# Optimization experiments

Hardware: AMD Instinct MI355X
Metric: run time of the kernel (lower is better)

## Reference

```python
import jax, jax.numpy as jnp
import numpy as np

BS, NUM_PATCH, N_VARS, PATCH_LEN, D_MODEL = 32, 64, 321, 12, 128
TIME_RATIO, FREQ_RATIO = 0.5, 0.4


def setup_inputs() -> dict:
    key = jax.random.key(0)
    ks = jax.random.split(key, 7)
    x = jax.random.normal(ks[0], (BS, NUM_PATCH, N_VARS, PATCH_LEN), jnp.float32)
    W_in = jax.random.normal(ks[1], (PATCH_LEN, D_MODEL), jnp.float32) / np.sqrt(PATCH_LEN)
    b_in = jnp.zeros((D_MODEL,), jnp.float32)
    W_out = jax.random.normal(ks[2], (D_MODEL, PATCH_LEN), jnp.float32) / np.sqrt(D_MODEL)
    b_out = jnp.zeros((PATCH_LEN,), jnp.float32)
    # nn.Parameter(torch.zeros(1,1,1)) in the original; use small random scalars so grads are non-trivial
    time_mask_token = jax.random.normal(ks[3], (), jnp.float32) * 0.02
    freq_mask_token = jax.random.normal(ks[4], (), jnp.float32) * 0.02
    return {"x": x, "W_in": W_in, "b_in": b_in, "W_out": W_out, "b_out": b_out,
            "time_mask_token": time_mask_token, "freq_mask_token": freq_mask_token}


def _scatter_mask(idx, num_patch):
    # idx: [bs, n_vars, k] patch indices to mask (set False). Returns bool [bs, num_patch, n_vars].
    bs, nv, k = idx.shape
    m = jnp.ones((bs, num_patch, nv), dtype=bool)
    b = jnp.arange(bs)[:, None, None]
    v = jnp.arange(nv)[None, :, None]
    return m.at[b, idx, v].set(False)


def reference(x, W_in, b_in, W_out, b_out, time_mask_token, freq_mask_token):
    bs, num_patch, n_vars, patch_len = x.shape

    # patch2emb applied per token (equivalent to the gather-encode path since the
    # projection is pointwise per patch): [bs, np, nv, d_model]
    emb = jnp.einsum('bpvl,ld->bpvd', x, W_in) + b_in

    # ---- time masking: mask patches with highest coefficient of variation ----
    cv = jnp.std(x, axis=-1, ddof=1) / (jnp.mean(x, axis=-1) + 1e-6)  # [bs, np, nv]
    k_t = int(num_patch * TIME_RATIO)
    _, idx_t = jax.lax.top_k(jnp.transpose(cv, (0, 2, 1)), k_t)       # [bs, nv, k_t]
    mask_t = _scatter_mask(idx_t, num_patch)                           # True = keep
    tokens_t = jnp.where(mask_t[..., None], emb, time_mask_token)
    out_t = jnp.einsum('bpvd,dl->bpvl', tokens_t, W_out) + b_out

    # ---- freq masking: mask patches with lowest mean FFT magnitude ----
    mag = jnp.abs(jnp.fft.rfft(x, axis=-1))                            # [bs, np, nv, pl//2+1]
    score = mag.mean(axis=-1)                                          # [bs, np, nv]
    k_f = int(num_patch * FREQ_RATIO)
    _, idx_f = jax.lax.top_k(-jnp.transpose(score, (0, 2, 1)), k_f)    # smallest scores
    mask_f = _scatter_mask(idx_f, num_patch)
    tokens_f = jnp.where(mask_f[..., None], emb, freq_mask_token)
    out_f = jnp.einsum('bpvd,dl->bpvl', tokens_f, W_out) + b_out

    return out_t * 0.5 + out_f * 0.5
```

## Files before the change

### kernel.cpp

```cpp
#include <hip/hip_runtime.h>
#include <math.h>

constexpr int BS = 32, NV = 321, PL = 12, DM = 128;
constexpr int KT = 32;
constexpr int KF = 25;
constexpr int VB = 8;
constexpr int NCHUNK = 41;
constexpr int SST = 72;
constexpr int TOTPV = BS * 64 * NV;
constexpr int MASK_BYTE_OFF = 4096;

__device__ __forceinline__ unsigned ord(float f) {
  unsigned u = __float_as_uint(f);
  return ((int)u < 0) ? ~u : (u | 0x80000000u);
}

__global__ __launch_bounds__(512, 8) void score_kernel(
    const float* __restrict__ x, const float* __restrict__ W_in,
    const float* __restrict__ b_in, const float* __restrict__ W_out,
    const float* __restrict__ b_out, const float* __restrict__ tt,
    const float* __restrict__ ft, float* __restrict__ ws) {
  const int t = threadIdx.x;
  const int chunk = blockIdx.x;
  const int b = blockIdx.y;

  if (chunk == NCHUNK) {
    if (b != 0) return;
    if (t < 144) {
      const int l = t / 12, i = t % 12;
      const float4* Wi = (const float4*)(W_in + i * DM);
      float s = 0.f;
#pragma unroll 8
      for (int d4 = 0; d4 < 32; ++d4) {
        float4 a = Wi[d4];
        const float* wo = W_out + d4 * 48 + l;
        s += a.x * wo[0] + a.y * wo[12] + a.z * wo[24] + a.w * wo[36];
      }
      ws[t] = s;
    } else if (t < 168) {
      const int l = (t - 144) % 12;
      float cs = 0.f, cb = 0.f;
#pragma unroll 8
      for (int d = 0; d < DM; ++d) {
        float w = W_out[d * 12 + l];
        cs += w;
        cb += b_in[d] * w;
      }
      if (t < 156) {
        ws[144 + l] = cb;
        ws[156 + l] = tt[0] * cs;
      } else {
        ws[168 + l] = ft[0] * cs;
      }
    } else if (t < 180) {
      ws[180 + (t - 168)] = b_out[t - 168];
    }
    return;
  }

  __shared__ float scv[VB * SST];
  __shared__ float sfs[VB * SST];

  const int v0 = chunk * VB;
  const bool full = (chunk < 40);
  const int nv = full ? VB : 1;

  const float* xb = x + ((size_t)(b * 64) * NV + v0) * PL;

  int p, vv;
  bool valid;
  if (full) {
    p = t >> 3;
    vv = t & 7;
    valid = true;
  } else {
    p = t & 63;
    vv = 0;
    valid = (t < 64);
  }

  if (valid) {
    const float4* src = (const float4*)(xb + ((size_t)p * NV + vv) * PL);
    float4 a = src[0], bb = src[1], c = src[2];
    float xv[12];
    xv[0] = a.x;  xv[1] = a.y;  xv[2] = a.z;  xv[3] = a.w;
    xv[4] = bb.x; xv[5] = bb.y; xv[6] = bb.z; xv[7] = bb.w;
    xv[8] = c.x;  xv[9] = c.y;  xv[10] = c.z; xv[11] = c.w;

    float s = 0.f;
#pragma unroll
    for (int i = 0; i < 12; ++i) s += xv[i];
    const float m = s * (1.0f / 12.0f);
    float ss = 0.f;
#pragma unroll
    for (int i = 0; i < 12; ++i) {
      float d = xv[i] - m;
      ss += d * d;
    }
    const float cv = sqrtf(ss * (1.0f / 11.0f)) / (m + 1e-6f);

    const float H = 0.86602540378443864676f;
    const float e1 = xv[1] + xv[11], e2 = xv[2] + xv[10], e3 = xv[3] + xv[9],
                e4 = xv[4] + xv[8], e5 = xv[5] + xv[7];
    const float o1 = xv[1] - xv[11], o2 = xv[2] - xv[10], o3 = xv[3] - xv[9],
                o4 = xv[4] - xv[8], o5 = xv[5] - xv[7];
    float mag = fabsf(xv[0] + xv[6] + e1 + e2 + e3 + e4 + e5);
    float re = xv[0] - xv[6] + H * (e1 - e5) + 0.5f * (e2 - e4);
    float im = 0.5f * (o1 + o5) + H * (o2 + o4) + o3;
    mag += sqrtf(re * re + im * im);
    re = xv[0] + xv[6] + 0.5f * (e1 + e5) - 0.5f * (e2 + e4) - e3;
    im = H * (o1 + o2 - o4 - o5);
    mag += sqrtf(re * re + im * im);
    re = xv[0] - xv[6] - e2 + e4;
    im = o1 - o3 + o5;
    mag += sqrtf(re * re + im * im);
    re = xv[0] + xv[6] - 0.5f * (e1 + e2 + e4 + e5) + e3;
    im = H * (o1 - o2 + o4 - o5);
    mag += sqrtf(re * re + im * im);
    re = xv[0] - xv[6] + H * (e5 - e1) + 0.5f * (e2 - e4);
    im = 0.5f * (o1 + o5) - H * (o2 + o4) + o3;
    mag += sqrtf(re * re + im * im);
    re = xv[0] + xv[6] - e1 + e2 - e3 + e4 - e5;
    mag += fabsf(re);
    const float fs = mag * (1.0f / 7.0f);

    scv[vv * SST + p] = cv;
    sfs[vv * SST + p] = fs;
  }
  __syncthreads();

  const int wv = t >> 6, lane = t & 63;
  if (wv < nv) {
    const unsigned ut = ord(scv[wv * SST + lane]);
    const unsigned uf = ~ord(sfs[wv * SST + lane]);
    unsigned tht = 0, thf = 0;
#pragma unroll
    for (int bit = 31; bit >= 0; --bit) {
      const unsigned ct = tht | (1u << bit);
      const unsigned cf = thf | (1u << bit);
      const unsigned long long bt = __ballot(ut >= ct);
      const unsigned long long bf = __ballot(uf >= cf);
      if (__popcll(bt) >= KT) tht = ct;
      if (__popcll(bf) >= KF) thf = cf;
    }
    const unsigned long long pre = (1ull << lane) - 1ull;
    const int gt_t = __popcll(__ballot(ut > tht));
    const int rt = __popcll(__ballot(ut == tht) & pre);
    const bool masked_t = (ut > tht) || ((ut == tht) && (rt < KT - gt_t));
    const int gt_f = __popcll(__ballot(uf > thf));
    const int rf = __popcll(__ballot(uf == thf) & pre);
    const bool masked_f = (uf > thf) || ((uf == thf) && (rf < KF - gt_f));
    const unsigned long long bkt = __ballot(!masked_t);
    const unsigned long long bkf = __ballot(!masked_f);
    if (lane == 0) {
      unsigned long long* mk =
          (unsigned long long*)((char*)ws + MASK_BYTE_OFF);
      const int vidx = b * NV + v0 + wv;
      mk[2 * vidx] = bkt;
      mk[2 * vidx + 1] = bkf;
    }
  }
}

__global__ __launch_bounds__(256, 8) void decode_kernel(
    const float* __restrict__ x, const float* __restrict__ ws,
    float* __restrict__ out) {
  const int g = blockIdx.x * 256 + threadIdx.x;
  const unsigned v = (unsigned)g % NV;
  const unsigned bp = (unsigned)g / NV;
  const int p = bp & 63;
  const int b = bp >> 6;

  const float4* src = (const float4*)(x + (size_t)g * PL);
  float4 a = src[0], bb = src[1], c = src[2];
  float xv[12];
  xv[0] = a.x;  xv[1] = a.y;  xv[2] = a.z;  xv[3] = a.w;
  xv[4] = bb.x; xv[5] = bb.y; xv[6] = bb.z; xv[7] = bb.w;
  xv[8] = c.x;  xv[9] = c.y;  xv[10] = c.z; xv[11] = c.w;

  const unsigned long long* mk =
      (const unsigned long long*)((const char*)ws + MASK_BYTE_OFF);
  const int vidx = b * NV + (int)v;
  const unsigned long long mT = mk[2 * vidx];
  const unsigned long long mF = mk[2 * vidx + 1];
  const bool kt = (mT >> p) & 1ull;
  const bool kf = (mF >> p) & 1ull;

  float o[12];
#pragma unroll
  for (int l0 = 0; l0 < 12; l0 += 4) {
#pragma unroll
    for (int l = l0; l < l0 + 4; ++l) {
      const float* Ml = ws + l * 12;
      float e = ws[144 + l];
#pragma unroll
      for (int i = 0; i < 12; ++i) e = fmaf(xv[i], Ml[i], e);
      const float at = kt ? e : ws[156 + l];
      const float af = kf ? e : ws[168 + l];
      o[l] = 0.5f * (at + af) + ws[180 + l];
    }
    if (l0 < 8) __builtin_amdgcn_sched_barrier(0);
  }

  float* op = out + (size_t)g * PL;
  ((float4*)op)[0] = make_float4(o[0], o[1], o[2], o[3]);
  ((float4*)op)[1] = make_float4(o[4], o[5], o[6], o[7]);
  ((float4*)op)[2] = make_float4(o[8], o[9], o[10], o[11]);
}

extern "C" void kernel_launch(void* const* d_in, const int* in_sizes, int n_in,
                              void* d_out, int out_size, void* d_ws,
                              size_t ws_size, hipStream_t stream) {
  const float* x = (const float*)d_in[0];
  const float* W_in = (const float*)d_in[1];
  const float* b_in = (const float*)d_in[2];
  const float* W_out = (const float*)d_in[3];
  const float* b_out = (const float*)d_in[4];
  const float* tt = (const float*)d_in[5];
  const float* ft = (const float*)d_in[6];
  float* out = (float*)d_out;
  float* ws = (float*)d_ws;

  hipLaunchKernelGGL(score_kernel, dim3(NCHUNK + 1, BS), dim3(512), 0, stream,
                     x, W_in, b_in, W_out, b_out, tt, ft, ws);
  hipLaunchKernelGGL(decode_kernel, dim3(TOTPV / 256), dim3(256), 0, stream, x,
                     ws, out);
}
```

Measured before the change: 110.0 us.

## Fuse scoring and decode into one kernel, keep masks in shared memory

Merges the score and decode kernels, so each block keeps its loaded x values in registers and its top-k masks in shared memory, then writes outputs directly. This removes the second full read of x and the global mask round trip. The weight prep moves to a separate single-block kernel launched first. The fused kernel has less parallelism per element: the last chunk uses only 64 of 512 threads, and output stores are strided per variable rather than fully contiguous.

```diff
diff --git a/kernel.cpp b/kernel.cpp
--- a/kernel.cpp
+++ b/kernel.cpp
@@ -7,60 +7,61 @@
 constexpr int VB = 8;
 constexpr int NCHUNK = 41;
 constexpr int SST = 72;
-constexpr int TOTPV = BS * 64 * NV;
-constexpr int MASK_BYTE_OFF = 4096;
 
 __device__ __forceinline__ unsigned ord(float f) {
   unsigned u = __float_as_uint(f);
   return ((int)u < 0) ? ~u : (u | 0x80000000u);
 }
 
-__global__ __launch_bounds__(512, 8) void score_kernel(
-    const float* __restrict__ x, const float* __restrict__ W_in,
-    const float* __restrict__ b_in, const float* __restrict__ W_out,
-    const float* __restrict__ b_out, const float* __restrict__ tt,
-    const float* __restrict__ ft, float* __restrict__ ws) {
+__global__ void prep_kernel(const float* __restrict__ W_in,
+                            const float* __restrict__ b_in,
+                            const float* __restrict__ W_out,
+                            const float* __restrict__ b_out,
+                            const float* __restrict__ tt,
+                            const float* __restrict__ ft,
+                            float* __restrict__ ws) {
+  const int t = threadIdx.x;
+  if (t < 144) {
+    const int l = t / 12, i = t % 12;
+    const float4* Wi = (const float4*)(W_in + i * DM);
+    float s = 0.f;
+#pragma unroll 8
+    for (int d4 = 0; d4 < 32; ++d4) {
+      float4 a = Wi[d4];
+      const float* wo = W_out + d4 * 48 + l;
+      s += a.x * wo[0] + a.y * wo[12] + a.z * wo[24] + a.w * wo[36];
+    }
+    ws[t] = s;
+  } else if (t < 168) {
+    const int l = (t - 144) % 12;
+    float cs = 0.f, cb = 0.f;
+#pragma unroll 8
+    for (int d = 0; d < DM; ++d) {
+      float w = W_out[d * 12 + l];
+      cs += w;
+      cb += b_in[d] * w;
+    }
+    if (t < 156) {
+      ws[144 + l] = cb;
+      ws[156 + l] = tt[0] * cs;
+    } else {
+      ws[168 + l] = ft[0] * cs;
+    }
+  } else if (t < 180) {
+    ws[180 + (t - 168)] = b_out[t - 168];
+  }
+}
+
+__global__ __launch_bounds__(512, 8) void fused_kernel(
+    const float* __restrict__ x, const float* __restrict__ prep,
+    float* __restrict__ out) {
+  __shared__ float scv[VB * SST];
+  __shared__ float sfs[VB * SST];
+  __shared__ unsigned long long smT[VB], smF[VB];
+
   const int t = threadIdx.x;
   const int chunk = blockIdx.x;
   const int b = blockIdx.y;
-
-  if (chunk == NCHUNK) {
-    if (b != 0) return;
-    if (t < 144) {
-      const int l = t / 12, i = t % 12;
-      const float4* Wi = (const float4*)(W_in + i * DM);
-      float s = 0.f;
-#pragma unroll 8
-      for (int d4 = 0; d4 < 32; ++d4) {
-        float4 a = Wi[d4];
-        const float* wo = W_out + d4 * 48 + l;
-        s += a.x * wo[0] + a.y * wo[12] + a.z * wo[24] + a.w * wo[36];
-      }
-      ws[t] = s;
-    } else if (t < 168) {
-      const int l = (t - 144) % 12;
-      float cs = 0.f, cb = 0.f;
-#pragma unroll 8
-      for (int d = 0; d < DM; ++d) {
-        float w = W_out[d * 12 + l];
-        cs += w;
-        cb += b_in[d] * w;
-      }
-      if (t < 156) {
-        ws[144 + l] = cb;
-        ws[156 + l] = tt[0] * cs;
-      } else {
-        ws[168 + l] = ft[0] * cs;
-      }
-    } else if (t < 180) {
-      ws[180 + (t - 168)] = b_out[t - 168];
-    }
-    return;
-  }
-
-  __shared__ float scv[VB * SST];
-  __shared__ float sfs[VB * SST];
-
   const int v0 = chunk * VB;
   const bool full = (chunk < 40);
   const int nv = full ? VB : 1;
@@ -79,10 +80,10 @@
     valid = (t < 64);
   }
 
+  float xv[12];
   if (valid) {
     const float4* src = (const float4*)(xb + ((size_t)p * NV + vv) * PL);
     float4 a = src[0], bb = src[1], c = src[2];
-    float xv[12];
     xv[0] = a.x;  xv[1] = a.y;  xv[2] = a.z;  xv[3] = a.w;
     xv[4] = bb.x; xv[5] = bb.y; xv[6] = bb.z; xv[7] = bb.w;
     xv[8] = c.x;  xv[9] = c.y;  xv[10] = c.z; xv[11] = c.w;
@@ -153,59 +154,35 @@
     const unsigned long long bkt = __ballot(!masked_t);
     const unsigned long long bkf = __ballot(!masked_f);
     if (lane == 0) {
-      unsigned long long* mk =
-          (unsigned long long*)((char*)ws + MASK_BYTE_OFF);
-      const int vidx = b * NV + v0 + wv;
-      mk[2 * vidx] = bkt;
-      mk[2 * vidx + 1] = bkf;
-    }
-  }
-}
-
-__global__ __launch_bounds__(256, 8) void decode_kernel(
-    const float* __restrict__ x, const float* __restrict__ ws,
-    float* __restrict__ out) {
-  const int g = blockIdx.x * 256 + threadIdx.x;
-  const unsigned v = (unsigned)g % NV;
-  const unsigned bp = (unsigned)g / NV;
-  const int p = bp & 63;
-  const int b = bp >> 6;
-
-  const float4* src = (const float4*)(x + (size_t)g * PL);
-  float4 a = src[0], bb = src[1], c = src[2];
-  float xv[12];
-  xv[0] = a.x;  xv[1] = a.y;  xv[2] = a.z;  xv[3] = a.w;
-  xv[4] = bb.x; xv[5] = bb.y; xv[6] = bb.z; xv[7] = bb.w;
-  xv[8] = c.x;  xv[9] = c.y;  xv[10] = c.z; xv[11] = c.w;
-
-  const unsigned long long* mk =
-      (const unsigned long long*)((const char*)ws + MASK_BYTE_OFF);
-  const int vidx = b * NV + (int)v;
-  const unsigned long long mT = mk[2 * vidx];
-  const unsigned long long mF = mk[2 * vidx + 1];
-  const bool kt = (mT >> p) & 1ull;
-  const bool kf = (mF >> p) & 1ull;
-
-  float o[12];
-#pragma unroll
-  for (int l0 = 0; l0 < 12; l0 += 4) {
-#pragma unroll
-    for (int l = l0; l < l0 + 4; ++l) {
-      const float* Ml = ws + l * 12;
-      float e = ws[144 + l];
-#pragma unroll
-      for (int i = 0; i < 12; ++i) e = fmaf(xv[i], Ml[i], e);
-      const float at = kt ? e : ws[156 + l];
-      const float af = kf ? e : ws[168 + l];
-      o[l] = 0.5f * (at + af) + ws[180 + l];
-    }
-    if (l0 < 8) __builtin_amdgcn_sched_barrier(0);
-  }
-
-  float* op = out + (size_t)g * PL;
-  ((float4*)op)[0] = make_float4(o[0], o[1], o[2], o[3]);
-  ((float4*)op)[1] = make_float4(o[4], o[5], o[6], o[7]);
-  ((float4*)op)[2] = make_float4(o[8], o[9], o[10], o[11]);
+      smT[wv] = bkt;
+      smF[wv] = bkf;
+    }
+  }
+  __syncthreads();
+
+  if (valid) {
+    const bool kt = (smT[vv] >> p) & 1ull;
+    const bool kf = (smF[vv] >> p) & 1ull;
+    float o[12];
+#pragma unroll
+    for (int l0 = 0; l0 < 12; l0 += 4) {
+#pragma unroll
+      for (int l = l0; l < l0 + 4; ++l) {
+        const float* Ml = prep + l * 12;
+        float e = prep[144 + l];
+#pragma unroll
+        for (int i = 0; i < 12; ++i) e = fmaf(xv[i], Ml[i], e);
+        const float at = kt ? e : prep[156 + l];
+        const float af = kf ? e : prep[168 + l];
+        o[l] = 0.5f * (at + af) + prep[180 + l];
+      }
+      if (l0 < 8) __builtin_amdgcn_sched_barrier(0);
+    }
+    float* op = out + ((size_t)(b * 64 + p) * NV + v0 + vv) * PL;
+    ((float4*)op)[0] = make_float4(o[0], o[1], o[2], o[3]);
+    ((float4*)op)[1] = make_float4(o[4], o[5], o[6], o[7]);
+    ((float4*)op)[2] = make_float4(o[8], o[9], o[10], o[11]);
+  }
 }
 
 extern "C" void kernel_launch(void* const* d_in, const int* in_sizes, int n_in,
@@ -221,8 +198,8 @@
   float* out = (float*)d_out;
   float* ws = (float*)d_ws;
 
-  hipLaunchKernelGGL(score_kernel, dim3(NCHUNK + 1, BS), dim3(512), 0, stream,
-                     x, W_in, b_in, W_out, b_out, tt, ft, ws);
-  hipLaunchKernelGGL(decode_kernel, dim3(TOTPV / 256), dim3(256), 0, stream, x,
+  hipLaunchKernelGGL(prep_kernel, dim3(1), dim3(192), 0, stream, W_in, b_in,
+                     W_out, b_out, tt, ft, ws);
+  hipLaunchKernelGGL(fused_kernel, dim3(NCHUNK, BS), dim3(512), 0, stream, x,
                      ws, out);
 }
```

After: 112.3 us. 1.02x slower.
